# Kernel tuning notes

Measured on AMD Instinct MI355X. Metric: run time of the kernel, lower is better.

## Reference

```python
import jax, jax.numpy as jnp
import numpy as np

# ---- constants mirroring tinyRSNN __init__ ----
DT = 0.004
THRESHOLD = 1.0
SOFTPLUS_1 = float(np.log1p(np.e))  # softplus(1.0) = 1.3132617
TAU_SYN_H = SOFTPLUS_1 * 0.01
TAU_MEM_H = SOFTPLUS_1 * 0.02
TAU_SYN_O = SOFTPLUS_1 * 0.01
TAU_MEM_O = SOFTPLUS_1 * 0.02

T, B, IN, H, OUT = 4096, 128, 96, 64, 2


def setup_inputs() -> dict:
    key = jax.random.key(0)
    k0, k1, k2, k3 = jax.random.split(key, 4)
    x = jax.random.normal(k0, (T, B, IN), dtype=jnp.float32)
    W_h = jax.random.normal(k1, (H, IN), dtype=jnp.float32) / np.sqrt(IN)
    V = jax.random.normal(k2, (H, H), dtype=jnp.float32) / np.sqrt(H)
    W_o = jax.random.normal(k3, (OUT, H), dtype=jnp.float32) / np.sqrt(H)
    return {"x": x, "W_h": W_h, "V": V, "W_o": W_o}


def _spike(u):
    # forward: Heaviside(u); surrogate gradient handled in fwdbwd module
    return (u > 0).astype(u.dtype)


def reference(x, W_h, V, W_o):
    # exponential decay factors (stork-like synaptic/membrane dynamics)
    alpha_h = jnp.exp(-DT / TAU_SYN_H)
    beta_h = jnp.exp(-DT / TAU_MEM_H)
    alpha_o = jnp.exp(-DT / TAU_SYN_O)
    beta_o = jnp.exp(-DT / TAU_MEM_O)

    def step(carry, x_t):
        prev_inp, spk, syn, mem, syn_o, mem_o = carry
        # NOTE: module feeds the PREVIOUS input and PREVIOUS hidden spikes
        cur_h = prev_inp @ W_h.T                       # [B,H]
        syn = alpha_h * syn + cur_h + spk @ V.T        # synaptic current
        mem = beta_h * mem + (1.0 - beta_h) * syn      # membrane integration
        new_spk = _spike(mem - THRESHOLD)              # threshold at 1
        mem = mem * (1.0 - new_spk)                    # reset_mechanism='zero'
        # readout LIF (reset_mechanism='none'), driven by previous spikes
        syn_o = alpha_o * syn_o + spk @ W_o.T
        mem_o = beta_o * mem_o + (1.0 - beta_o) * syn_o
        return (x_t, new_spk, syn, mem, syn_o, mem_o), mem_o

    z = lambda *s: jnp.zeros(s, dtype=x.dtype)
    init = (z(B, IN), z(B, H), z(B, H), z(B, H), z(B, OUT), z(B, OUT))
    _, preds = jax.lax.scan(step, init, x)             # preds: [T,B,OUT]
    return preds
```

## Files before the change

kernel.cpp:

```cpp
#include <hip/hip_runtime.h>
#include <cmath>

#define T_STEPS 4096
#define BATCH   128
#define NIN     96
#define NH      64

typedef unsigned short u16;

__device__ __forceinline__ float bf2f(u16 u) {
    unsigned v = ((unsigned)u) << 16;
    return __builtin_bit_cast(float, v);
}
__device__ __forceinline__ double d_alpha() { return exp(-0.004 / (log1p(exp(1.0)) * 0.01)); }
__device__ __forceinline__ double d_beta()  { return exp(-0.004 / (log1p(exp(1.0)) * 0.02)); }

__device__ __forceinline__ int sniff_part(const void* p, int nscan, int tid, int nthr) {
    const u16* q = (const u16*)p;
    int cnt = 0;
    for (int i = tid; i < nscan; i += nthr) {
        float v = bf2f(q[i]);
        if (!(fabsf(v) < 1e4f)) cnt++;
    }
    return cnt;
}
__device__ __forceinline__ int wave_sum(int c) {
#pragma unroll
    for (int d = 32; d >= 1; d >>= 1) c += __shfl_xor(c, d, 64);
    return c;
}

__device__ __forceinline__ void acc_chunk(float* __restrict__ acc,
                                          const float* __restrict__ xr,
                                          const float* __restrict__ wbase) {
#pragma unroll
    for (int h = 0; h < 64; ++h) {
        const float4* wr = (const float4*)(wbase + h * NIN);
        const float4 w0 = wr[0], w1 = wr[1], w2 = wr[2], w3 = wr[3];
        float c = acc[h];
        c = fmaf(xr[0],  w0.x, c); c = fmaf(xr[1],  w0.y, c);
        c = fmaf(xr[2],  w0.z, c); c = fmaf(xr[3],  w0.w, c);
        c = fmaf(xr[4],  w1.x, c); c = fmaf(xr[5],  w1.y, c);
        c = fmaf(xr[6],  w1.z, c); c = fmaf(xr[7],  w1.w, c);
        c = fmaf(xr[8],  w2.x, c); c = fmaf(xr[9],  w2.y, c);
        c = fmaf(xr[10], w2.z, c); c = fmaf(xr[11], w2.w, c);
        c = fmaf(xr[12], w3.x, c); c = fmaf(xr[13], w3.y, c);
        c = fmaf(xr[14], w3.z, c); c = fmaf(xr[15], w3.w, c);
        acc[h] = c;
    }
}

__global__ __launch_bounds__(256) void k_cur(const void* __restrict__ xv,
                                             const void* __restrict__ whv,
                                             float* __restrict__ cur) {
    const int NROWC = (T_STEPS - 1) * BATCH;
    const int tid = threadIdx.x;
    __shared__ int s_cnt[2];
    __shared__ __align__(16) float whs[NH * NIN];
    if (tid < 2) s_cnt[tid] = 0;
    __syncthreads();
    int c0 = sniff_part(xv, 512, tid, 256);
    int c1 = sniff_part(whv, 512, tid, 256);
    if (c0) atomicAdd(&s_cnt[0], c0);
    if (c1) atomicAdd(&s_cnt[1], c1);
    __syncthreads();
    const bool fx = s_cnt[0] >= 32, fw = s_cnt[1] >= 32;

    if (fw) {
        const float* w = (const float*)whv;
        for (int s = tid; s < NH * NIN; s += 256) whs[s] = w[s];
    } else {
        const u16* w = (const u16*)whv;
        for (int s = tid; s < NH * NIN; s += 256) whs[s] = bf2f(w[s]);
    }
    __syncthreads();

    const long r = (long)blockIdx.x * 256 + tid;
    if (r >= NROWC) {
        const long z = r - NROWC;
        if (z < BATCH) {
            float4 zero = {0.f, 0.f, 0.f, 0.f};
            float4* zp = (float4*)(cur + z * NH);
#pragma unroll
            for (int j = 0; j < 16; ++j) zp[j] = zero;
        }
        return;
    }

    float acc[64];
#pragma unroll
    for (int h = 0; h < 64; ++h) acc[h] = 0.f;

    if (!fx) {
        const uint4* xq = (const uint4*)((const u16*)xv + (size_t)r * NIN);
        uint4 n0 = xq[0], n1 = xq[1];
#pragma unroll 1
        for (int kb = 0; kb < 6; ++kb) {
            const uint4 a = n0, b = n1;
            if (kb < 5) { n0 = xq[(kb + 1) * 2]; n1 = xq[(kb + 1) * 2 + 1]; }
            const unsigned ua[8] = {a.x, a.y, a.z, a.w, b.x, b.y, b.z, b.w};
            float xr[16];
#pragma unroll
            for (int j = 0; j < 8; ++j) {
                xr[2 * j]     = bf2f((u16)(ua[j] & 0xFFFFu));
                xr[2 * j + 1] = bf2f((u16)(ua[j] >> 16));
            }
            acc_chunk(acc, xr, whs + kb * 16);
        }
    } else {
        const float4* xq = (const float4*)((const float*)xv + (size_t)r * NIN);
        float4 n0 = xq[0], n1 = xq[1], n2 = xq[2], n3 = xq[3];
#pragma unroll 1
        for (int kb = 0; kb < 6; ++kb) {
            const float4 a0 = n0, a1 = n1, a2 = n2, a3 = n3;
            if (kb < 5) {
                n0 = xq[(kb + 1) * 4];     n1 = xq[(kb + 1) * 4 + 1];
                n2 = xq[(kb + 1) * 4 + 2]; n3 = xq[(kb + 1) * 4 + 3];
            }
            const float xr[16] = {a0.x, a0.y, a0.z, a0.w, a1.x, a1.y, a1.z, a1.w,
                                  a2.x, a2.y, a2.z, a2.w, a3.x, a3.y, a3.z, a3.w};
            acc_chunk(acc, xr, whs + kb * 16);
        }
    }

    float4* op = (float4*)(cur + ((size_t)r + BATCH) * NH);
#pragma unroll
    for (int j = 0; j < 16; ++j) {
        float4 v;
        v.x = acc[4 * j]; v.y = acc[4 * j + 1]; v.z = acc[4 * j + 2]; v.w = acc[4 * j + 3];
        op[j] = v;
    }
}

__global__ __launch_bounds__(64, 1) void k_scan(const float* __restrict__ cur,
                                                const void* __restrict__ vv,
                                                _Float16* __restrict__ ftr) {
    const int b = blockIdx.x, h = threadIdx.x;
    const double alpha = d_alpha(), beta = d_beta(), ombeta = 1.0 - beta;
    const float alphaf = (float)alpha, betaf = (float)beta, ombetaf = (float)ombeta;

    const bool fv = wave_sum(sniff_part(vv, 512, h, 64)) >= 32;

    __shared__ float vlds[NH * NH];
    if (fv) {
        const float* vp = (const float*)vv;
        for (int s = h; s < NH * NH; s += 64) vlds[((s & 63) << 6) | (s >> 6)] = vp[s];
    } else {
        const u16* vp = (const u16*)vv;
        for (int s = h; s < NH * NH; s += 64) vlds[((s & 63) << 6) | (s >> 6)] = bf2f(vp[s]);
    }
    __syncthreads();

    double syn = 0.0, mem = 0.0;
    float e = 0.f, f = 0.f, spkf = 0.f;
    unsigned long long mask = 0ull;

    const size_t STEP = (size_t)BATCH * NH;
    const float* cp = cur + (size_t)b * NH + h;
    _Float16* fp = ftr + (size_t)b * NH + h;

    float cbuf[8];
#pragma unroll
    for (int j = 0; j < 8; ++j) cbuf[j] = cp[(size_t)j * STEP];

    for (int tt = 0; tt < T_STEPS; tt += 8) {
#pragma unroll
        for (int j = 0; j < 8; ++j) {
            const float c = cbuf[j];
            int tn = tt + j + 8;
            if (tn > T_STEPS - 1) tn = T_STEPS - 1;
            cbuf[j] = cp[(size_t)tn * STEP];

            double rec = 0.0;
            unsigned long long m = mask;
            while (m) {
                const int k = __builtin_ctzll(m);
                m &= m - 1;
                rec += (double)vlds[(k << 6) | h];
            }

            syn = alpha * syn + ((double)c + rec);
            mem = beta * mem + ombeta * syn;

            e = fmaf(alphaf, e, spkf);
            f = fmaf(betaf, f, ombetaf * e);
            fp[(size_t)(tt + j) * STEP] = (_Float16)f;

            const bool s = mem > 1.0;
            mem = s ? 0.0 : mem;
            spkf = s ? 1.0f : 0.0f;
            mask = __ballot(s);
        }
    }
}

__global__ __launch_bounds__(256) void k_out(const _Float16* __restrict__ ftr,
                                             const void* __restrict__ wov,
                                             float* __restrict__ out) {
    const int tid = threadIdx.x;
    const bool fo = sniff_part(wov, 120, 0, 1) >= 7;
    __shared__ float wo[2][64];
    if (fo) {
        if (tid < 128) wo[tid >> 6][tid & 63] = ((const float*)wov)[tid];
    } else {
        if (tid < 128) wo[tid >> 6][tid & 63] = bf2f(((const u16*)wov)[tid]);
    }
    __syncthreads();

    const size_t idx = (size_t)blockIdx.x * 256 + tid;
    const unsigned* up = (const unsigned*)(ftr + idx * NH);
    float d0 = 0.f, d1 = 0.f;
#pragma unroll
    for (int j = 0; j < 32; ++j) {
        const unsigned u = up[j];
        const float f0 = (float)__builtin_bit_cast(_Float16, (unsigned short)(u & 0xFFFFu));
        const float f1 = (float)__builtin_bit_cast(_Float16, (unsigned short)(u >> 16));
        d0 = fmaf(f0, wo[0][2 * j], d0);
        d1 = fmaf(f0, wo[1][2 * j], d1);
        d0 = fmaf(f1, wo[0][2 * j + 1], d0);
        d1 = fmaf(f1, wo[1][2 * j + 1], d1);
    }
    float2 r; r.x = d0; r.y = d1;
    ((float2*)out)[idx] = r;
}

__global__ __launch_bounds__(64) void k_fused(const void* __restrict__ xv,
                                              const void* __restrict__ whv,
                                              const void* __restrict__ vv,
                                              const void* __restrict__ wov,
                                              float* __restrict__ out) {
    const int b = blockIdx.x, h = threadIdx.x;
    const double alpha = d_alpha(), beta = d_beta(), ombeta = 1.0 - beta;

    const bool fx = wave_sum(sniff_part(xv, 512, h, 64)) >= 32;
    const bool fw = wave_sum(sniff_part(whv, 512, h, 64)) >= 32;
    const bool fv = wave_sum(sniff_part(vv, 512, h, 64)) >= 32;
    const bool fo = wave_sum(sniff_part(wov, 120, h, 64)) >= 7;

    __shared__ float vlds[NH * NH];
    __shared__ float whl[NIN * NH];
    if (fv) { const float* vp = (const float*)vv;
        for (int s = h; s < NH * NH; s += 64) vlds[((s & 63) << 6) | (s >> 6)] = vp[s]; }
    else    { const u16* vp = (const u16*)vv;
        for (int s = h; s < NH * NH; s += 64) vlds[((s & 63) << 6) | (s >> 6)] = bf2f(vp[s]); }
    if (fw) { const float* wp = (const float*)whv;
        for (int s = h; s < NH * NIN; s += 64) whl[(s % 96) * 64 + (s / 96)] = wp[s]; }
    else    { const u16* wp = (const u16*)whv;
        for (int s = h; s < NH * NIN; s += 64) whl[(s % 96) * 64 + (s / 96)] = bf2f(wp[s]); }
    __syncthreads();

    double wo0, wo1;
    if (fo) { wo0 = (double)((const float*)wov)[h]; wo1 = (double)((const float*)wov)[64 + h]; }
    else    { wo0 = (double)bf2f(((const u16*)wov)[h]); wo1 = (double)bf2f(((const u16*)wov)[64 + h]); }

    double syn = 0.0, mem = 0.0, syno0 = 0.0, memo0 = 0.0, syno1 = 0.0, memo1 = 0.0;
    double spkd = 0.0;
    unsigned long long mask = 0ull;

    for (int t = 0; t < T_STEPS; ++t) {
        float c = 0.0f;
        if (t > 0) {
            const size_t off = ((size_t)(t - 1) * BATCH + b) * NIN;
            if (fx) { const float* xp = (const float*)xv + off;
                for (int i = 0; i < NIN; ++i) c = fmaf(xp[i], whl[i * 64 + h], c); }
            else    { const u16* xp = (const u16*)xv + off;
                for (int i = 0; i < NIN; ++i) c = fmaf(bf2f(xp[i]), whl[i * 64 + h], c); }
        }
        double rec = 0.0;
        unsigned long long m = mask;
        while (m) { const int k = __builtin_ctzll(m); m &= m - 1; rec += (double)vlds[(k << 6) | h]; }

        syn = alpha * syn + ((double)c + rec);
        mem = beta * mem + ombeta * syn;

        double p0 = spkd * wo0, p1 = spkd * wo1;
#pragma unroll
        for (int d = 32; d >= 1; d >>= 1) { p0 += __shfl_xor(p0, d, 64); p1 += __shfl_xor(p1, d, 64); }
        syno0 = alpha * syno0 + p0;
        memo0 = beta * memo0 + ombeta * syno0;
        syno1 = alpha * syno1 + p1;
        memo1 = beta * memo1 + ombeta * syno1;
        if (h == 0) {
            const size_t w = ((size_t)t * BATCH + b) * 2;
            out[w] = (float)memo0;
            out[w + 1] = (float)memo1;
        }

        const bool s = mem > 1.0;
        mem = s ? 0.0 : mem;
        spkd = s ? 1.0 : 0.0;
        mask = __ballot(s);
    }
}

extern "C" void kernel_launch(void* const* d_in, const int* in_sizes, int n_in,
                              void* d_out, int out_size, void* d_ws, size_t ws_size,
                              hipStream_t stream) {
    (void)in_sizes; (void)out_size;
    if (n_in < 4) return;
    const void* x  = d_in[0];
    const void* Wh = d_in[1];
    const void* V  = d_in[2];
    const void* Wo = d_in[3];
    float* out = (float*)d_out;

    const size_t NROW = (size_t)T_STEPS * BATCH;
    const size_t curB = NROW * NH * sizeof(float);
    const size_t ftrB = NROW * NH * sizeof(_Float16);

    if (ws_size >= curB + ftrB) {
        float* cur = (float*)d_ws;
        _Float16* ftr = (_Float16*)((char*)d_ws + curB);
        const int NBLK = (int)(NROW / 256);
        k_cur<<<NBLK, 256, 0, stream>>>(x, Wh, cur);
        k_scan<<<BATCH, 64, 0, stream>>>(cur, V, ftr);
        k_out<<<NROW / 256, 256, 0, stream>>>(ftr, Wo, out);
    } else {
        k_fused<<<BATCH, 64, 0, stream>>>(x, Wh, V, Wo, out);
    }
}
```

Measured before the change: 946.9 us.

## Shorten scan critical path and stage readout loads through padded LDS

In the serial scan, the spike decision is rewritten algebraically as fma(ombeta, rec, pre) > 1 - beta*mem. This lets the terms that do not depend on the recurrent sum be computed before the ballot-dependent gather. The first eight recurrent-weight gathers are issued independently, using a zero sentinel row at index 64, and reduced as a tree instead of a serial chain. The readout kernel now loads its block's fp16 traces with coalesced reads into a padded LDS tile rather than strided per-thread global reads. The spike comparison can differ from the old one in rare rounding cases, and more LDS is used.

```diff
diff --git a/kernel.cpp b/kernel.cpp
--- a/kernel.cpp
+++ b/kernel.cpp
@@ -141,7 +141,7 @@
 
     const bool fv = wave_sum(sniff_part(vv, 512, h, 64)) >= 32;
 
-    __shared__ float vlds[NH * NH];
+    __shared__ float vlds[65 * NH];
     if (fv) {
         const float* vp = (const float*)vv;
         for (int s = h; s < NH * NH; s += 64) vlds[((s & 63) << 6) | (s >> 6)] = vp[s];
@@ -149,6 +149,7 @@
         const u16* vp = (const u16*)vv;
         for (int s = h; s < NH * NH; s += 64) vlds[((s & 63) << 6) | (s >> 6)] = bf2f(vp[s]);
     }
+    vlds[(64 << 6) | h] = 0.0f;
     __syncthreads();
 
     double syn = 0.0, mem = 0.0;
@@ -171,13 +172,38 @@
             if (tn > T_STEPS - 1) tn = T_STEPS - 1;
             cbuf[j] = cp[(size_t)tn * STEP];
 
+            const double pre = ombeta * fma(alpha, syn, (double)c);
+            const double rhs = 1.0 - beta * mem;
+
             double rec = 0.0;
             unsigned long long m = mask;
-            while (m) {
-                const int k = __builtin_ctzll(m);
-                m &= m - 1;
-                rec += (double)vlds[(k << 6) | h];
+            if (m) {
+                const int k0 = (int)__builtin_ctzll(m); m &= m - 1;
+                const int k1 = m ? (int)__builtin_ctzll(m) : 64; m &= m - 1;
+                const int k2 = m ? (int)__builtin_ctzll(m) : 64; m &= m - 1;
+                const int k3 = m ? (int)__builtin_ctzll(m) : 64; m &= m - 1;
+                const int k4 = m ? (int)__builtin_ctzll(m) : 64; m &= m - 1;
+                const int k5 = m ? (int)__builtin_ctzll(m) : 64; m &= m - 1;
+                const int k6 = m ? (int)__builtin_ctzll(m) : 64; m &= m - 1;
+                const int k7 = m ? (int)__builtin_ctzll(m) : 64; m &= m - 1;
+                const float r0 = vlds[(k0 << 6) | h];
+                const float r1 = vlds[(k1 << 6) | h];
+                const float r2 = vlds[(k2 << 6) | h];
+                const float r3 = vlds[(k3 << 6) | h];
+                const float r4 = vlds[(k4 << 6) | h];
+                const float r5 = vlds[(k5 << 6) | h];
+                const float r6 = vlds[(k6 << 6) | h];
+                const float r7 = vlds[(k7 << 6) | h];
+                rec = (((double)r0 + (double)r1) + ((double)r2 + (double)r3))
+                    + (((double)r4 + (double)r5) + ((double)r6 + (double)r7));
+                while (m) {
+                    const int k = (int)__builtin_ctzll(m);
+                    m &= m - 1;
+                    rec += (double)vlds[(k << 6) | h];
+                }
             }
+
+            const bool s = fma(ombeta, rec, pre) > rhs;
 
             syn = alpha * syn + ((double)c + rec);
             mem = beta * mem + ombeta * syn;
@@ -186,7 +212,6 @@
             f = fmaf(betaf, f, ombetaf * e);
             fp[(size_t)(tt + j) * STEP] = (_Float16)f;
 
-            const bool s = mem > 1.0;
             mem = s ? 0.0 : mem;
             spkf = s ? 1.0f : 0.0f;
             mask = __ballot(s);
@@ -198,17 +223,25 @@
                                              const void* __restrict__ wov,
                                              float* __restrict__ out) {
     const int tid = threadIdx.x;
+    __shared__ unsigned tile[256 * 34];
+    __shared__ float wo[2][64];
     const bool fo = sniff_part(wov, 120, 0, 1) >= 7;
-    __shared__ float wo[2][64];
     if (fo) {
         if (tid < 128) wo[tid >> 6][tid & 63] = ((const float*)wov)[tid];
     } else {
         if (tid < 128) wo[tid >> 6][tid & 63] = bf2f(((const u16*)wov)[tid]);
     }
+
+    const unsigned* src = (const unsigned*)(ftr + (size_t)blockIdx.x * 256 * NH);
+#pragma unroll
+    for (int i = 0; i < 32; ++i) {
+        const int s = i * 256 + tid;
+        tile[(s >> 5) * 34 + (s & 31)] = src[s];
+    }
     __syncthreads();
 
     const size_t idx = (size_t)blockIdx.x * 256 + tid;
-    const unsigned* up = (const unsigned*)(ftr + idx * NH);
+    const unsigned* up = &tile[tid * 34];
     float d0 = 0.f, d1 = 0.f;
 #pragma unroll
     for (int j = 0; j < 32; ++j) {
```

Result: slower. 1.180 ms (+24.6%).
